# Performance work log

Measured on AMD Instinct MI355X. Metric: run time of the kernel, lower is better.

## Reference

```python
import jax, jax.numpy as jnp
import numpy as np


def setup_inputs() -> dict:
    key = jax.random.key(0)
    k1, k2, k3, k4 = jax.random.split(key, 4)
    B, S, D = 64, 4096, 256
    return {
        "enc_out": jax.random.normal(k1, (B, S, D), dtype=jnp.float32),
        "We_w": jax.random.normal(k2, (1, D), dtype=jnp.float32) * (1.0 / np.sqrt(D)),
        "We_b": jax.random.normal(k3, (1,), dtype=jnp.float32) * 0.01,
        "ut_w": jax.random.normal(k4, (1, 1), dtype=jnp.float32),
    }


def reference(enc_out, We_w, We_b, ut_w):
    # enc_out: [B, S, D]. Per-timestep score: u_t(W_e(enc_out)) -> scalar per (s, b).
    # Vectorized form of the original python loop (score is computed once, not S times).
    scores = (jnp.einsum("bsd,d->bs", enc_out, We_w[0]) + We_b[0]) * ut_w[0, 0]  # [B, S]
    # F.softmax on the [S, B, 1] tensor defaults to dim 0 (the seq dim).
    w = jax.nn.softmax(scores, axis=1)  # [B, S]
    # enc_out.transpose(0,2) * tgtweight summed over seq -> [D, B]
    out = jnp.einsum("bsd,bs->db", enc_out, w)
    return out
```

## Files before the change

kernel.cpp:

```cpp
#include <hip/hip_runtime.h>
#include <math.h>

#define B_ 64
#define S_ 4096
#define D_ 256
#define SPLITS 32
#define ROWS_PER_BLOCK (S_ / SPLITS)
#define NWAVES 4
#define ROWS_PER_WAVE (ROWS_PER_BLOCK / NWAVES)
#define NPART (B_ * SPLITS)

__global__ __launch_bounds__(256) void ta_partial(
    const float* __restrict__ enc, const float* __restrict__ We_w,
    const float* __restrict__ We_b, const float* __restrict__ ut_w,
    float* __restrict__ ws)
{
    const int blk   = blockIdx.x;
    const int b     = blk >> 5;
    const int split = blk & (SPLITS - 1);
    const int tid   = threadIdx.x;
    const int wave  = tid >> 6;
    const int lane  = tid & 63;

    const float4 w4  = reinterpret_cast<const float4*>(We_w)[lane];
    const float bias = We_b[0];
    const float ut   = ut_w[0];

    const float* rowbase = enc +
        ((size_t)b * S_ + (size_t)split * ROWS_PER_BLOCK +
         (size_t)wave * ROWS_PER_WAVE) * D_;

    float m = -INFINITY, l = 0.0f;
    float ax = 0.0f, ay = 0.0f, az = 0.0f, aw = 0.0f;

    #pragma unroll 2
    for (int r = 0; r < ROWS_PER_WAVE; ++r) {
        const float4 v =
            reinterpret_cast<const float4*>(rowbase + (size_t)r * D_)[lane];
        float dot = v.x * w4.x;
        dot = fmaf(v.y, w4.y, dot);
        dot = fmaf(v.z, w4.z, dot);
        dot = fmaf(v.w, w4.w, dot);
        #pragma unroll
        for (int mask = 32; mask >= 1; mask >>= 1)
            dot += __shfl_xor(dot, mask, 64);
        const float s  = (dot + bias) * ut;
        const float mn = fmaxf(m, s);
        if (mn > m) {
            const float c = __expf(m - mn);
            l *= c; ax *= c; ay *= c; az *= c; aw *= c;
            m = mn;
        }
        const float p = __expf(s - m);
        l += p;
        ax = fmaf(p, v.x, ax);
        ay = fmaf(p, v.y, ay);
        az = fmaf(p, v.z, az);
        aw = fmaf(p, v.w, aw);
    }

    __shared__ float  sm[NWAVES], sl[NWAVES];
    __shared__ float4 sacc[NWAVES][64];
    sacc[wave][lane] = make_float4(ax, ay, az, aw);
    if (lane == 0) { sm[wave] = m; sl[wave] = l; }
    __syncthreads();

    const float M  = fmaxf(fmaxf(sm[0], sm[1]), fmaxf(sm[2], sm[3]));
    const float f0 = __expf(sm[0] - M), f1 = __expf(sm[1] - M);
    const float f2 = __expf(sm[2] - M), f3 = __expf(sm[3] - M);
    const float L  = f0 * sl[0] + f1 * sl[1] + f2 * sl[2] + f3 * sl[3];

    const float* sa = reinterpret_cast<const float*>(&sacc[0][0]);
    const float av = f0 * sa[0 * D_ + tid] + f1 * sa[1 * D_ + tid] +
                     f2 * sa[2 * D_ + tid] + f3 * sa[3 * D_ + tid];

    float* ws_acc = ws;
    float* ws_m   = ws + (size_t)NPART * D_;
    float* ws_l   = ws_m + NPART;
    ws_acc[(size_t)blk * D_ + tid] = av;
    if (tid == 0) { ws_m[blk] = M; ws_l[blk] = L; }
}

__global__ __launch_bounds__(256) void ta_reduce(
    const float* __restrict__ ws, float* __restrict__ out)
{
    const int b = blockIdx.x;
    const int d = threadIdx.x;
    const float* ws_acc = ws;
    const float* ws_m   = ws + (size_t)NPART * D_;
    const float* ws_l   = ws_m + NPART;

    float M = -INFINITY;
    #pragma unroll
    for (int i = 0; i < SPLITS; ++i)
        M = fmaxf(M, ws_m[b * SPLITS + i]);

    float L = 0.0f, acc = 0.0f;
    #pragma unroll 4
    for (int i = 0; i < SPLITS; ++i) {
        const int p   = b * SPLITS + i;
        const float f = __expf(ws_m[p] - M);
        L   += f * ws_l[p];
        acc  = fmaf(f, ws_acc[(size_t)p * D_ + d], acc);
    }
    out[(size_t)d * B_ + b] = acc / L;
}

extern "C" void kernel_launch(void* const* d_in, const int* in_sizes, int n_in,
                              void* d_out, int out_size, void* d_ws, size_t ws_size,
                              hipStream_t stream)
{
    const float* enc  = (const float*)d_in[0];
    const float* We_w = (const float*)d_in[1];
    const float* We_b = (const float*)d_in[2];
    const float* ut_w = (const float*)d_in[3];
    float* out = (float*)d_out;
    float* ws  = (float*)d_ws;

    ta_partial<<<NPART, 256, 0, stream>>>(enc, We_w, We_b, ut_w, ws);
    ta_reduce<<<B_, 256, 0, stream>>>(ws, out);
}
```

Measured before the change: 361.8 us.

## Batch rows by eight with register double-buffering and transposed shuffle reduction

Processes rows in batches of eight, prefetching the next batch into a register double buffer so global loads overlap compute. The eight per-row dot products are reduced together with a butterfly transpose (8+4+2 shuffles then 3 more) instead of six shuffles per row, and scores are broadcast via readlane. The online softmax rescale is done once per batch instead of per row. This raises register use, which may lower occupancy.

After: 360.9 us. About the same (-0.2%).

```diff
diff --git a/kernel.cpp b/kernel.cpp
--- a/kernel.cpp
+++ b/kernel.cpp
@@ -8,7 +8,12 @@
 #define ROWS_PER_BLOCK (S_ / SPLITS)
 #define NWAVES 4
 #define ROWS_PER_WAVE (ROWS_PER_BLOCK / NWAVES)
+#define NBATCH (ROWS_PER_WAVE / 8)
 #define NPART (B_ * SPLITS)
+
+__device__ __forceinline__ float bcast(float x, int srcLane) {
+    return __int_as_float(__builtin_amdgcn_readlane(__float_as_int(x), srcLane));
+}
 
 __global__ __launch_bounds__(256) void ta_partial(
     const float* __restrict__ enc, const float* __restrict__ We_w,
@@ -30,33 +35,89 @@
         ((size_t)b * S_ + (size_t)split * ROWS_PER_BLOCK +
          (size_t)wave * ROWS_PER_WAVE) * D_;
 
+    const bool h1 = lane & 1, h2 = lane & 2, h3 = lane & 4;
+
     float m = -INFINITY, l = 0.0f;
     float ax = 0.0f, ay = 0.0f, az = 0.0f, aw = 0.0f;
 
-    #pragma unroll 2
-    for (int r = 0; r < ROWS_PER_WAVE; ++r) {
-        const float4 v =
-            reinterpret_cast<const float4*>(rowbase + (size_t)r * D_)[lane];
-        float dot = v.x * w4.x;
-        dot = fmaf(v.y, w4.y, dot);
-        dot = fmaf(v.z, w4.z, dot);
-        dot = fmaf(v.w, w4.w, dot);
+    float4 buf[2][8];
+    #pragma unroll
+    for (int r = 0; r < 8; ++r)
+        buf[0][r] = reinterpret_cast<const float4*>(rowbase + (size_t)r * D_)[lane];
+
+    #pragma unroll
+    for (int bt = 0; bt < NBATCH; ++bt) {
+        const int cur = bt & 1, nxt = cur ^ 1;
+        if (bt < NBATCH - 1) {
+            #pragma unroll
+            for (int r = 0; r < 8; ++r)
+                buf[nxt][r] = reinterpret_cast<const float4*>(
+                    rowbase + (size_t)((bt + 1) * 8 + r) * D_)[lane];
+        }
+
+        float pd[8];
         #pragma unroll
-        for (int mask = 32; mask >= 1; mask >>= 1)
-            dot += __shfl_xor(dot, mask, 64);
-        const float s  = (dot + bias) * ut;
-        const float mn = fmaxf(m, s);
-        if (mn > m) {
-            const float c = __expf(m - mn);
-            l *= c; ax *= c; ay *= c; az *= c; aw *= c;
-            m = mn;
+        for (int r = 0; r < 8; ++r) {
+            const float4 v = buf[cur][r];
+            float d = v.x * w4.x;
+            d = fmaf(v.y, w4.y, d);
+            d = fmaf(v.z, w4.z, d);
+            d = fmaf(v.w, w4.w, d);
+            pd[r] = d;
         }
-        const float p = __expf(s - m);
-        l += p;
-        ax = fmaf(p, v.x, ax);
-        ay = fmaf(p, v.y, ay);
-        az = fmaf(p, v.z, az);
-        aw = fmaf(p, v.w, aw);
+
+        float q[4];
+        #pragma unroll
+        for (int k = 0; k < 4; ++k) {
+            const float send = h1 ? pd[k] : pd[k + 4];
+            const float keep = h1 ? pd[k + 4] : pd[k];
+            q[k] = keep + __shfl_xor(send, 1, 64);
+        }
+        float u[2];
+        #pragma unroll
+        for (int k = 0; k < 2; ++k) {
+            const float send = h2 ? q[k] : q[k + 2];
+            const float keep = h2 ? q[k + 2] : q[k];
+            u[k] = keep + __shfl_xor(send, 2, 64);
+        }
+        float t;
+        {
+            const float send = h3 ? u[0] : u[1];
+            const float keep = h3 ? u[1] : u[0];
+            t = keep + __shfl_xor(send, 4, 64);
+        }
+        t += __shfl_xor(t, 8, 64);
+        t += __shfl_xor(t, 16, 64);
+        t += __shfl_xor(t, 32, 64);
+
+        float s[8];
+        s[0] = (bcast(t, 0) + bias) * ut;
+        s[1] = (bcast(t, 4) + bias) * ut;
+        s[2] = (bcast(t, 2) + bias) * ut;
+        s[3] = (bcast(t, 6) + bias) * ut;
+        s[4] = (bcast(t, 1) + bias) * ut;
+        s[5] = (bcast(t, 5) + bias) * ut;
+        s[6] = (bcast(t, 3) + bias) * ut;
+        s[7] = (bcast(t, 7) + bias) * ut;
+
+        float pm = s[0];
+        #pragma unroll
+        for (int r = 1; r < 8; ++r) pm = fmaxf(pm, s[r]);
+        const float mn = fmaxf(m, pm);
+        const float c  = __expf(m - mn);
+        m = mn;
+        l *= c; ax *= c; ay *= c; az *= c; aw *= c;
+
+        #pragma unroll
+        for (int r = 0; r < 8; ++r) {
+            const float p = __expf(s[r] - mn);
+            const float4 v = buf[cur][r];
+            l  += p;
+            ax  = fmaf(p, v.x, ax);
+            ay  = fmaf(p, v.y, ay);
+            az  = fmaf(p, v.z, az);
+            aw  = fmaf(p, v.w, aw);
+        }
     }
 
     __shared__ float  sm[NWAVES], sl[NWAVES];
```
